# Performance work log

Measured on AMD Instinct MI355X. Metric: run time of the kernel, lower is better.

The kernel has to match this reference:

```python
import jax, jax.numpy as jnp
import numpy as np

TEMPERATURE = 0.7
BIG_NEG = -1e30  # safe stand-in for -inf (keeps grads finite)


def setup_inputs() -> dict:
    key = jax.random.key(0)
    k1, k2, k3 = jax.random.split(key, 3)
    B, D = 8192, 256
    embeddings = jax.random.normal(k1, (B, D), dtype=jnp.float32)
    categories = jax.random.randint(k2, (B,), 0, 16, dtype=jnp.int64)
    font_labels = jax.random.randint(k3, (B,), 0, 2000, dtype=jnp.int64)
    return {"embeddings": embeddings, "categories": categories, "font_labels": font_labels}


def reference(embeddings, categories, font_labels):
    # L2-normalize rows
    e = embeddings / jnp.linalg.norm(embeddings, axis=1, keepdims=True)
    sims = jnp.matmul(e, e.T) / TEMPERATURE  # [B, B]
    B = sims.shape[0]

    same = categories[:, None] == categories[None, :]
    diag = jnp.eye(B, dtype=bool)
    pos_mask = same & ~diag           # same category, excluding self
    neg_mask = ~same                  # different category (self excluded implicitly)

    valid = pos_mask.any(axis=1) & neg_mask.any(axis=1)

    pos_sim = jnp.max(jnp.where(pos_mask, sims, BIG_NEG), axis=1)  # hardest positive per anchor
    neg_max = jnp.max(jnp.where(neg_mask, sims, BIG_NEG), axis=1)

    # logsumexp over {pos_sim} U neg_sims, numerically stable
    m = jnp.where(valid, jnp.maximum(pos_sim, neg_max), 0.0)
    pos_safe = jnp.where(valid, pos_sim, 0.0)
    exp_neg_sum = jnp.sum(jnp.where(neg_mask, jnp.exp(sims - m[:, None]), 0.0), axis=1)
    lse = m + jnp.log(jnp.exp(pos_safe - m) + exp_neg_sum)

    loss_per_anchor = -pos_safe + lse
    n_valid = jnp.maximum(jnp.sum(valid), 1)
    return jnp.sum(jnp.where(valid, loss_per_anchor, 0.0)) / n_valid
```

## Files before the change

### kernel.cpp

```cpp
#include <hip/hip_runtime.h>
#include <stdint.h>

#define NROWS 8192
#define DDIM 256
#define NSTRIPS 16
#define STRIP_COLS 512
#define BN 32
#define NTILES 16
#define BM 128

#define ESCALE 1.4356159f
#define LN2F   0.6931471806f
#define NEGBIG (-1e30f)

typedef __attribute__((ext_vector_type(8))) short short8;
typedef __attribute__((ext_vector_type(4))) float f32x4;

typedef __attribute__((address_space(3))) void lds_void;
typedef const __attribute__((address_space(1))) void gl_void;

__device__ __forceinline__ unsigned short f2bf(float x) {
  unsigned int u = __float_as_uint(x);
  u += 0x7fffu + ((u >> 16) & 1u);
  return (unsigned short)(u >> 16);
}

__global__ __launch_bounds__(256) void knorm(const float* __restrict__ emb,
                                             unsigned short* __restrict__ ebf) {
  const int wave = threadIdx.x >> 6, lane = threadIdx.x & 63;
  const int row = blockIdx.x * 4 + wave;
  const float4 v = *(const float4*)(emb + row * DDIM + lane * 4);
  float ss = v.x * v.x + v.y * v.y + v.z * v.z + v.w * v.w;
#pragma unroll
  for (int off = 1; off < 64; off <<= 1) ss += __shfl_xor(ss, off, 64);
  const float sc = rsqrtf(ss) * ESCALE;
  ushort4 o;
  o.x = f2bf(v.x * sc); o.y = f2bf(v.y * sc);
  o.z = f2bf(v.z * sc); o.w = f2bf(v.w * sc);
  *(ushort4*)(ebf + row * DDIM + lane * 4) = o;
}

__global__ __launch_bounds__(256) void kmain(const unsigned short* __restrict__ ebf,
                                             const int* __restrict__ cats,
                                             float* __restrict__ posP,
                                             float* __restrict__ sumP) {
  __shared__ alignas(16) unsigned short smem[2][BN * DDIM];
  const int tid = threadIdx.x;
  const int lane = tid & 63, wave = tid >> 6;
  const int lane15 = lane & 15, quad = lane >> 4;
  const int strip = blockIdx.x, rowTile = blockIdx.y;
  const int rowG = rowTile * BM + wave * 32;
  const int col0 = strip * STRIP_COLS;

  short8 a[2][8];
#pragma unroll
  for (int m = 0; m < 2; ++m)
#pragma unroll
    for (int kk = 0; kk < 8; ++kk)
      a[m][kk] = *(const short8*)(ebf + (rowG + m * 16 + lane15) * DDIM + kk * 32 + quad * 8);

  int cati[2][4];
#pragma unroll
  for (int m = 0; m < 2; ++m)
#pragma unroll
    for (int r = 0; r < 4; ++r)
      cati[m][r] = cats[rowG + m * 16 + quad * 4 + r];

  bool dlr[4];
#pragma unroll
  for (int r = 0; r < 4; ++r) dlr[r] = (lane15 == quad * 4 + r);

  float pm[2][4], ns[2][4];
#pragma unroll
  for (int m = 0; m < 2; ++m)
#pragma unroll
    for (int r = 0; r < 4; ++r) { pm[m][r] = NEGBIG; ns[m][r] = 0.f; }

#define STAGE(t, buf)                                                           \
  {                                                                             \
    const unsigned short* g = ebf +                                             \
        (size_t)(col0 + (t) * BN + (lane & 31)) * DDIM +                        \
        (wave * 2 + (lane >> 5)) * 8;                                           \
    char* lb = (char*)&smem[(buf)][0] + wave * 1024;                            \
    _Pragma("unroll")                                                           \
    for (int c = 0; c < 4; ++c)                                                 \
      __builtin_amdgcn_global_load_lds((gl_void*)(g + c * 64),                  \
                                       (lds_void*)(lb + c * 4096), 16, 0, 0);   \
  }

  STAGE(0, 0);

  for (int t = 0; t < NTILES; ++t) {
    __syncthreads();
    if (t + 1 < NTILES) STAGE(t + 1, (t + 1) & 1);
    const char* bb = (const char*)&smem[t & 1][0];
    const int colBase = col0 + t * BN;
    const int cjt[2] = {cats[colBase + lane15], cats[colBase + 16 + lane15]};

#pragma unroll
    for (int nt = 0; nt < 2; ++nt) {
      short8 b[8];
#pragma unroll
      for (int kk = 0; kk < 8; ++kk)
        b[kk] = *(const short8*)(bb + kk * 2048 + quad * 512 + nt * 256 + lane15 * 16);
      f32x4 acc0 = {0.f, 0.f, 0.f, 0.f}, acc1 = {0.f, 0.f, 0.f, 0.f};
      __builtin_amdgcn_s_setprio(1);
#pragma unroll
      for (int kk = 0; kk < 8; ++kk) {
        acc0 = __builtin_amdgcn_mfma_f32_16x16x32_bf16(a[0][kk], b[kk], acc0, 0, 0, 0);
        acc1 = __builtin_amdgcn_mfma_f32_16x16x32_bf16(a[1][kk], b[kk], acc1, 0, 0, 0);
      }
      __builtin_amdgcn_s_setprio(0);
      const int cj = cjt[nt];
      const bool dg0 = (rowG == colBase + nt * 16);
      const bool dg1 = (rowG + 16 == colBase + nt * 16);
#pragma unroll
      for (int m = 0; m < 2; ++m) {
        const bool dg = m ? dg1 : dg0;
#pragma unroll
        for (int r = 0; r < 4; ++r) {
          const float s = m ? acc1[r] : acc0[r];
          const float e = __builtin_amdgcn_exp2f(s);
          const bool same = (cj == cati[m][r]);
          float psv = same ? s : NEGBIG;
          if (dg) psv = dlr[r] ? NEGBIG : psv;
          pm[m][r] = fmaxf(pm[m][r], psv);
          ns[m][r] += same ? 0.f : e;
        }
      }
    }
  }

#pragma unroll
  for (int off = 1; off < 16; off <<= 1) {
#pragma unroll
    for (int m = 0; m < 2; ++m)
#pragma unroll
      for (int r = 0; r < 4; ++r) {
        pm[m][r] = fmaxf(pm[m][r], __shfl_xor(pm[m][r], off, 64));
        ns[m][r] += __shfl_xor(ns[m][r], off, 64);
      }
  }
  if (lane15 == 0) {
#pragma unroll
    for (int m = 0; m < 2; ++m)
#pragma unroll
      for (int r = 0; r < 4; ++r) {
        const int row = rowG + m * 16 + quad * 4 + r;
        posP[strip * NROWS + row] = pm[m][r];
        sumP[strip * NROWS + row] = ns[m][r];
      }
  }
}

__global__ __launch_bounds__(256) void kmerge(const float* __restrict__ posP,
                                              const float* __restrict__ sumP,
                                              float* __restrict__ acc,
                                              float* __restrict__ out) {
  const int row = blockIdx.x * 256 + threadIdx.x;
  float pm = NEGBIG, ns = 0.f;
#pragma unroll
  for (int s = 0; s < NSTRIPS; ++s) {
    pm = fmaxf(pm, posP[s * NROWS + row]);
    ns += sumP[s * NROWS + row];
  }
  const bool valid = (pm > -1e29f) && (ns > 0.f);
  float loss = valid ? (logf(__builtin_amdgcn_exp2f(pm) + ns) - pm * LN2F) : 0.f;
  float cnt = valid ? 1.f : 0.f;
#pragma unroll
  for (int off = 1; off < 64; off <<= 1) {
    loss += __shfl_xor(loss, off, 64);
    cnt += __shfl_xor(cnt, off, 64);
  }
  if ((threadIdx.x & 63) == 0) {
    atomicAdd(&acc[0], loss);
    atomicAdd(&acc[1], cnt);
    __threadfence();
  }
  __syncthreads();
  if (threadIdx.x == 0) {
    const int prev = atomicAdd((int*)(acc + 2), 1);
    if (prev == (int)gridDim.x - 1) {
      const float L = atomicAdd(&acc[0], 0.f);
      const float C = atomicAdd(&acc[1], 0.f);
      out[0] = L / fmaxf(C, 1.f);
    }
  }
}

extern "C" void kernel_launch(void* const* d_in, const int* in_sizes, int n_in,
                              void* d_out, int out_size, void* d_ws, size_t ws_size,
                              hipStream_t stream) {
  const float* emb = (const float*)d_in[0];
  const int* cats = (const int*)d_in[1];
  float* out = (float*)d_out;

  char* ws = (char*)d_ws;
  float* accv = (float*)ws;
  unsigned short* ebf = (unsigned short*)(ws + 256);
  float* posP = (float*)(ws + 256 + NROWS * DDIM * 2);
  float* sumP = posP + NSTRIPS * NROWS;

  hipMemsetAsync(accv, 0, 16, stream);
  knorm<<<NROWS / 4, 256, 0, stream>>>(emb, ebf);
  kmain<<<dim3(NSTRIPS, NROWS / BM), 256, 0, stream>>>(ebf, cats, posP, sumP);
  kmerge<<<NROWS / 256, 256, 0, stream>>>(posP, sumP, accv, out);
}
```

Measured before the change: 118.3 us.

## Fuse merge into main kernel via atomics and last-block reduction

Removes the separate merge kernel and the memset. Workspace zeroing moves into block 0 of the normalize kernel. The main kernel now combines per-strip partials through atomicMax on order-preserving float keys and atomicAdd on sums, and the last block to finish computes the final loss. This cuts two launches and the partials round trip, but adds global atomic contention and a serial tail reduction done by a single block.

```diff
diff --git a/kernel.cpp b/kernel.cpp
--- a/kernel.cpp
+++ b/kernel.cpp
@@ -8,10 +8,16 @@
 #define BN 32
 #define NTILES 16
 #define BM 128
+#define NBLOCKS (NSTRIPS * (NROWS / BM))
 
 #define ESCALE 1.4356159f
 #define LN2F   0.6931471806f
 #define NEGBIG (-1e30f)
+
+#define WS_PMK   256
+#define WS_NS    (256 + 32768)
+#define WS_EBF   (256 + 65536)
+#define WS_ZERO_BYTES (256 + 65536)
 
 typedef __attribute__((ext_vector_type(8))) short short8;
 typedef __attribute__((ext_vector_type(4))) float f32x4;
@@ -25,8 +31,22 @@
   return (unsigned short)(u >> 16);
 }
 
+__device__ __forceinline__ unsigned fkey(float f) {
+  unsigned b = __float_as_uint(f);
+  return (b & 0x80000000u) ? ~b : (b | 0x80000000u);
+}
+__device__ __forceinline__ float funkey(unsigned k) {
+  unsigned b = (k & 0x80000000u) ? (k & 0x7fffffffu) : ~k;
+  return __uint_as_float(b);
+}
+
 __global__ __launch_bounds__(256) void knorm(const float* __restrict__ emb,
-                                             unsigned short* __restrict__ ebf) {
+                                             unsigned short* __restrict__ ebf,
+                                             uint4* __restrict__ zbase) {
+  if (blockIdx.x == 0) {
+    const uint4 z = {0u, 0u, 0u, 0u};
+    for (int i = threadIdx.x; i < WS_ZERO_BYTES / 16; i += 256) zbase[i] = z;
+  }
   const int wave = threadIdx.x >> 6, lane = threadIdx.x & 63;
   const int row = blockIdx.x * 4 + wave;
   const float4 v = *(const float4*)(emb + row * DDIM + lane * 4);
@@ -42,9 +62,13 @@
 
 __global__ __launch_bounds__(256) void kmain(const unsigned short* __restrict__ ebf,
                                              const int* __restrict__ cats,
-                                             float* __restrict__ posP,
-                                             float* __restrict__ sumP) {
+                                             unsigned* __restrict__ pmk,
+                                             float* __restrict__ nsum,
+                                             int* __restrict__ cnt,
+                                             float* __restrict__ out) {
   __shared__ alignas(16) unsigned short smem[2][BN * DDIM];
+  __shared__ int isLast;
+  __shared__ float red[8];
   const int tid = threadIdx.x;
   const int lane = tid & 63, wave = tid >> 6;
   const int lane15 = lane & 15, quad = lane >> 4;
@@ -147,42 +171,37 @@
 #pragma unroll
       for (int r = 0; r < 4; ++r) {
         const int row = rowG + m * 16 + quad * 4 + r;
-        posP[strip * NROWS + row] = pm[m][r];
-        sumP[strip * NROWS + row] = ns[m][r];
-      }
-  }
-}
-
-__global__ __launch_bounds__(256) void kmerge(const float* __restrict__ posP,
-                                              const float* __restrict__ sumP,
-                                              float* __restrict__ acc,
-                                              float* __restrict__ out) {
-  const int row = blockIdx.x * 256 + threadIdx.x;
-  float pm = NEGBIG, ns = 0.f;
-#pragma unroll
-  for (int s = 0; s < NSTRIPS; ++s) {
-    pm = fmaxf(pm, posP[s * NROWS + row]);
-    ns += sumP[s * NROWS + row];
-  }
-  const bool valid = (pm > -1e29f) && (ns > 0.f);
-  float loss = valid ? (logf(__builtin_amdgcn_exp2f(pm) + ns) - pm * LN2F) : 0.f;
-  float cnt = valid ? 1.f : 0.f;
-#pragma unroll
-  for (int off = 1; off < 64; off <<= 1) {
-    loss += __shfl_xor(loss, off, 64);
-    cnt += __shfl_xor(cnt, off, 64);
-  }
-  if ((threadIdx.x & 63) == 0) {
-    atomicAdd(&acc[0], loss);
-    atomicAdd(&acc[1], cnt);
+        atomicMax(&pmk[row], fkey(pm[m][r]));
+        atomicAdd(&nsum[row], ns[m][r]);
+      }
     __threadfence();
   }
   __syncthreads();
-  if (threadIdx.x == 0) {
-    const int prev = atomicAdd((int*)(acc + 2), 1);
-    if (prev == (int)gridDim.x - 1) {
-      const float L = atomicAdd(&acc[0], 0.f);
-      const float C = atomicAdd(&acc[1], 0.f);
+  if (tid == 0) {
+    const int prev = atomicAdd(cnt, 1);
+    isLast = (prev == NBLOCKS - 1);
+  }
+  __syncthreads();
+  if (isLast) {
+    float lsum = 0.f, csum = 0.f;
+    for (int i = tid; i < NROWS; i += 256) {
+      const unsigned k = atomicOr(&pmk[i], 0u);
+      const float nsv = atomicAdd(&nsum[i], 0.f);
+      const float pmv = funkey(k);
+      const bool valid = (pmv > -1e29f) && (nsv > 0.f);
+      lsum += valid ? (logf(__builtin_amdgcn_exp2f(pmv) + nsv) - pmv * LN2F) : 0.f;
+      csum += valid ? 1.f : 0.f;
+    }
+#pragma unroll
+    for (int off = 1; off < 64; off <<= 1) {
+      lsum += __shfl_xor(lsum, off, 64);
+      csum += __shfl_xor(csum, off, 64);
+    }
+    if (lane == 0) { red[wave * 2] = lsum; red[wave * 2 + 1] = csum; }
+    __syncthreads();
+    if (tid == 0) {
+      const float L = red[0] + red[2] + red[4] + red[6];
+      const float C = red[1] + red[3] + red[5] + red[7];
       out[0] = L / fmaxf(C, 1.f);
     }
   }
@@ -196,13 +215,11 @@
   float* out = (float*)d_out;
 
   char* ws = (char*)d_ws;
-  float* accv = (float*)ws;
-  unsigned short* ebf = (unsigned short*)(ws + 256);
-  float* posP = (float*)(ws + 256 + NROWS * DDIM * 2);
-  float* sumP = posP + NSTRIPS * NROWS;
-
-  hipMemsetAsync(accv, 0, 16, stream);
-  knorm<<<NROWS / 4, 256, 0, stream>>>(emb, ebf);
-  kmain<<<dim3(NSTRIPS, NROWS / BM), 256, 0, stream>>>(ebf, cats, posP, sumP);
-  kmerge<<<NROWS / 256, 256, 0, stream>>>(posP, sumP, accv, out);
-}
+  int* cnt = (int*)ws;
+  unsigned* pmk = (unsigned*)(ws + WS_PMK);
+  float* nsum = (float*)(ws + WS_NS);
+  unsigned short* ebf = (unsigned short*)(ws + WS_EBF);
+
+  knorm<<<NROWS / 4, 256, 0, stream>>>(emb, ebf, (uint4*)ws);
+  kmain<<<dim3(NSTRIPS, NROWS / BM), 256, 0, stream>>>(ebf, cats, pmk, nsum, cnt, out);
+}
```

New measurement: 190.4 us. +60.9%, slower.

## Exploit similarity matrix symmetry by computing only upper-triangular 128x128 blocks

Applied to the files above, without the earlier changes.

The main kernel now tiles the Gram matrix into 128x128 blocks and skips blocks below the diagonal. Each off-diagonal block also reduces its results column-wise through shared memory, so every block yields partial max and exp-sums for both its row block and its column block. This roughly halves the MFMA and exp work. In exchange it adds 64 partial slots per row, which makes the merge kernel read much more data, and it launches a 64x64 grid in which half the blocks exit immediately.

```diff
diff --git a/kernel.cpp b/kernel.cpp
--- a/kernel.cpp
+++ b/kernel.cpp
@@ -3,11 +3,11 @@
 
 #define NROWS 8192
 #define DDIM 256
-#define NSTRIPS 16
-#define STRIP_COLS 512
+#define RB 128
+#define NRB (NROWS / RB)
 #define BN 32
-#define NTILES 16
-#define BM 128
+#define NTILES (RB / BN)
+#define NSLOT NRB
 
 #define ESCALE 1.4356159f
 #define LN2F   0.6931471806f
@@ -44,13 +44,16 @@
                                              const int* __restrict__ cats,
                                              float* __restrict__ posP,
                                              float* __restrict__ sumP) {
+  const int I = blockIdx.y, J = blockIdx.x;
+  if (J < I) return;
   __shared__ alignas(16) unsigned short smem[2][BN * DDIM];
+  __shared__ float cpm[4][RB], cns[4][RB];
   const int tid = threadIdx.x;
   const int lane = tid & 63, wave = tid >> 6;
   const int lane15 = lane & 15, quad = lane >> 4;
-  const int strip = blockIdx.x, rowTile = blockIdx.y;
-  const int rowG = rowTile * BM + wave * 32;
-  const int col0 = strip * STRIP_COLS;
+  const bool offd = (I != J);
+  const int rowG = I * RB + wave * 32;
+  const int col0 = J * RB;
 
   short8 a[2][8];
 #pragma unroll
@@ -114,6 +117,7 @@
       const int cj = cjt[nt];
       const bool dg0 = (rowG == colBase + nt * 16);
       const bool dg1 = (rowG + 16 == colBase + nt * 16);
+      float cpmv = NEGBIG, cnsv = 0.f;
 #pragma unroll
       for (int m = 0; m < 2; ++m) {
         const bool dg = m ? dg1 : dg0;
@@ -125,7 +129,18 @@
           float psv = same ? s : NEGBIG;
           if (dg) psv = dlr[r] ? NEGBIG : psv;
           pm[m][r] = fmaxf(pm[m][r], psv);
-          ns[m][r] += same ? 0.f : e;
+          const float ev = same ? 0.f : e;
+          ns[m][r] += ev;
+          cpmv = fmaxf(cpmv, psv);
+          cnsv += ev;
+        }
+      }
+      if (offd) {
+        cpmv = fmaxf(cpmv, __shfl_xor(cpmv, 16, 64)); cnsv += __shfl_xor(cnsv, 16, 64);
+        cpmv = fmaxf(cpmv, __shfl_xor(cpmv, 32, 64)); cnsv += __shfl_xor(cnsv, 32, 64);
+        if (quad == 0) {
+          const int c = t * BN + nt * 16 + lane15;
+          cpm[wave][c] = cpmv; cns[wave][c] = cnsv;
         }
       }
     }
@@ -147,9 +162,19 @@
 #pragma unroll
       for (int r = 0; r < 4; ++r) {
         const int row = rowG + m * 16 + quad * 4 + r;
-        posP[strip * NROWS + row] = pm[m][r];
-        sumP[strip * NROWS + row] = ns[m][r];
-      }
+        posP[J * NROWS + row] = pm[m][r];
+        sumP[J * NROWS + row] = ns[m][r];
+      }
+  }
+  if (offd) {
+    __syncthreads();
+    if (tid < RB) {
+      const float p = fmaxf(fmaxf(cpm[0][tid], cpm[1][tid]),
+                            fmaxf(cpm[2][tid], cpm[3][tid]));
+      const float n = cns[0][tid] + cns[1][tid] + cns[2][tid] + cns[3][tid];
+      posP[I * NROWS + col0 + tid] = p;
+      sumP[I * NROWS + col0 + tid] = n;
+    }
   }
 }
 
@@ -159,8 +184,8 @@
                                               float* __restrict__ out) {
   const int row = blockIdx.x * 256 + threadIdx.x;
   float pm = NEGBIG, ns = 0.f;
-#pragma unroll
-  for (int s = 0; s < NSTRIPS; ++s) {
+#pragma unroll 8
+  for (int s = 0; s < NSLOT; ++s) {
     pm = fmaxf(pm, posP[s * NROWS + row]);
     ns += sumP[s * NROWS + row];
   }
@@ -199,10 +224,10 @@
   float* accv = (float*)ws;
   unsigned short* ebf = (unsigned short*)(ws + 256);
   float* posP = (float*)(ws + 256 + NROWS * DDIM * 2);
-  float* sumP = posP + NSTRIPS * NROWS;
+  float* sumP = posP + NSLOT * NROWS;
 
   hipMemsetAsync(accv, 0, 16, stream);
   knorm<<<NROWS / 4, 256, 0, stream>>>(emb, ebf);
-  kmain<<<dim3(NSTRIPS, NROWS / BM), 256, 0, stream>>>(ebf, cats, posP, sumP);
+  kmain<<<dim3(NRB, NRB), 256, 0, stream>>>(ebf, cats, posP, sumP);
   kmerge<<<NROWS / 256, 256, 0, stream>>>(posP, sumP, accv, out);
 }
```

Measured after the change: 141.2 us. 1.19x slower.
